# Optimization experiments

Hardware: AMD Instinct MI355X
Metric: run time of the kernel (lower is better)

The kernel has to match this reference:

```python
import jax, jax.numpy as jnp
import numpy as np

OUT_DIM = 336
ALPHA = 1000.0
BETA = 100.0
EPS = 1e-5


def _normalize(x, ref):
    # ref: [B,G,D] -> mean [B,G,1,D]; std is a GLOBAL scalar with ddof=1 (torch.std default)
    d = x - ref[:, :, None, :]
    std = jnp.std(d, ddof=1)
    return d / (std + EPS)


def _tr_embed(my_dim, T):
    # T: [B, in_dim, G, K] channel-first
    B, in_dim, G, K = T.shape
    fd = my_dim // (in_dim * 2)
    feat_range = jnp.arange(fd, dtype=T.dtype)
    dim_embed = jnp.power(jnp.asarray(ALPHA, T.dtype), feat_range / fd)  # [fd]
    t = jnp.transpose(T, (0, 2, 3, 1))                 # [B,G,K,in_dim]
    div = (BETA * t)[..., None] / dim_embed            # [B,G,K,in_dim,fd]
    e = jnp.stack([jnp.sin(div), jnpp_cos(div)], axis=4) if False else jnp.stack([jnp.sin(div), jnp.cos(div)], axis=4)  # [B,G,K,in_dim,2,fd]
    e = e.reshape(B, G, K, in_dim * 2 * fd)            # interleaved as (dim, sin/cos, feat)
    return jnp.transpose(e, (0, 3, 1, 2))              # [B, in_dim*2*fd, G, K]


def setup_inputs() -> dict:
    key = jax.random.key(0)
    k1, k2, k3, k4 = jax.random.split(key, 4)
    B, G, K, C = 8, 1024, 32, 168
    return {
        "lc_xyz": jax.random.normal(k1, (B, G, 3), dtype=jnp.float32),
        "lc_x": jax.random.normal(k2, (B, G, C), dtype=jnp.float32),
        "knn_xyz": jax.random.normal(k3, (B, G, K, 3), dtype=jnp.float32),
        "knn_x": jax.random.normal(k4, (B, G, K, C), dtype=jnp.float32),
    }


def reference(lc_xyz, lc_x, knn_xyz, knn_x):
    B, G, K, C = knn_x.shape
    knn_x_n = _normalize(knn_x, lc_x)          # [B,G,K,C]
    knn_xyz_n = _normalize(knn_xyz, lc_xyz)    # [B,G,K,3]

    lc = jnp.broadcast_to(lc_xyz[:, :, None, :], (B, G, K, 3))
    # channel-first layout as in the torch code
    knn_x_cf = jnp.transpose(knn_x_n, (0, 3, 1, 2))      # [B,C,G,K]
    knn_xyz_cf = jnp.transpose(knn_xyz_n, (0, 3, 1, 2))  # [B,3,G,K]
    lc_cf = jnp.transpose(lc, (0, 3, 1, 2))              # [B,3,G,K]

    cross = jnp.cross(knn_xyz_cf, lc_cf, axis=1)                        # [B,3,G,K]
    dot = jnp.sum(knn_xyz_cf * lc_cf, axis=1, keepdims=True)            # [B,1,G,K]
    emb = jnp.concatenate([knn_xyz_cf, cross, dot], axis=1)             # [B,7,G,K]
    emb = jnp.tile(emb, (1, C // 7, 1, 1))                              # [B,7*(C//7),G,K]
    knn_x_w = jnp.concatenate([knn_x_cf, emb], axis=1)                  # [B,2C,G,K]

    pe = _tr_embed(OUT_DIM, knn_xyz_cf) + _tr_embed(OUT_DIM, lc_cf)     # [B,OUT_DIM,G,K]
    return (knn_x_w + pe) * pe
```

## Files before the change

### kernel.cpp

```cpp
#include <hip/hip_runtime.h>

#define NGQ 1024
#define NKQ 32
#define NCQ 168
#define NOUTC 336
#define NXF 44040192
#define NXYZQ 786432
#define EPSV 1e-5f
#define PIO2 1.5707963267948966f
#define L2A_OVER_FD 0.17796043436f

#define NPART_X 1024
#define NPART_3 32
#define NPART (NPART_X + NPART_3)

#define GRID 512
#define TPB 512
#define NPAIR 4096
#define TSTR 169
#define TILEF (NKQ * TSTR)

__global__ __launch_bounds__(256) void reduce_kernel(
    const float* __restrict__ knn_x, const float* __restrict__ lc_x,
    const float* __restrict__ knn_xyz, const float* __restrict__ lc_xyz,
    float4* __restrict__ part)
{
    float s = 0.f, q = 0.f, s3 = 0.f, q3 = 0.f;
    const int blk = blockIdx.x;
    const int tid = threadIdx.x;

    if (blk < NPART_X) {
        const float4* __restrict__ x4 = (const float4*)knn_x;
        const int n4 = NXF / 4;
        for (int i = blk * 256 + tid; i < n4; i += NPART_X * 256) {
            float4 v = x4[i];
            int bg  = i / 1344;
            int c4  = i - bg * 1344;
            int r42 = c4 % 42;
            float4 l = *(const float4*)(lc_x + (size_t)bg * NCQ + r42 * 4);
            float dx = v.x - l.x, dy = v.y - l.y, dz = v.z - l.z, dw = v.w - l.w;
            s += (dx + dy) + (dz + dw);
            q = fmaf(dx, dx, q); q = fmaf(dy, dy, q);
            q = fmaf(dz, dz, q); q = fmaf(dw, dw, q);
        }
    } else {
        for (int i = (blk - NPART_X) * 256 + tid; i < NXYZQ; i += NPART_3 * 256) {
            float v = knn_xyz[i];
            int bg = i / 96;
            int j  = i % 3;
            float d = v - lc_xyz[bg * 3 + j];
            s3 += d;
            q3 = fmaf(d, d, q3);
        }
    }

    for (int off = 32; off; off >>= 1) {
        s  += __shfl_down(s,  off);
        q  += __shfl_down(q,  off);
        s3 += __shfl_down(s3, off);
        q3 += __shfl_down(q3, off);
    }
    __shared__ float red[4][4];
    int wv = tid >> 6;
    if ((tid & 63) == 0) { red[wv][0] = s; red[wv][1] = q; red[wv][2] = s3; red[wv][3] = q3; }
    __syncthreads();
    if (tid == 0) {
        part[blk] = make_float4(red[0][0] + red[1][0] + red[2][0] + red[3][0],
                                red[0][1] + red[1][1] + red[2][1] + red[3][1],
                                red[0][2] + red[1][2] + red[2][2] + red[3][2],
                                red[0][3] + red[1][3] + red[2][3] + red[3][3]);
    }
}

__global__ __launch_bounds__(TPB, 4) void main_kernel(
    const float* __restrict__ lc_xyz, const float* __restrict__ lc_x,
    const float* __restrict__ knn_xyz, const float* __restrict__ knn_x,
    const float4* __restrict__ part, float* __restrict__ out)
{
    __shared__ float  s_x[2 * TILEF];
    __shared__ float4 s_cc[2 * NOUTC];
    __shared__ float  s_emb[2 * NKQ * 7];
    __shared__ float2 s_so[NOUTC];
    __shared__ float  s_lc[6];
    __shared__ double redd[8][4];
    __shared__ float  s_inv[2];

    const int tid = threadIdx.x;
    const int wv  = tid >> 6;

    {
        double sd = 0.0, qd = 0.0, s3d = 0.0, q3d = 0.0;
        for (int i = tid; i < NPART; i += TPB) {
            float4 p = part[i];
            sd += p.x; qd += p.y; s3d += p.z; q3d += p.w;
        }
        for (int off = 32; off; off >>= 1) {
            sd  += __shfl_down(sd,  off);  qd  += __shfl_down(qd,  off);
            s3d += __shfl_down(s3d, off);  q3d += __shfl_down(q3d, off);
        }
        if ((tid & 63) == 0) { redd[wv][0]=sd; redd[wv][1]=qd; redd[wv][2]=s3d; redd[wv][3]=q3d; }
        __syncthreads();
        if (tid == 0) {
            double S=0,Q=0,S3=0,Q3=0;
            for (int w = 0; w < 8; ++w) { S+=redd[w][0]; Q+=redd[w][1]; S3+=redd[w][2]; Q3+=redd[w][3]; }
            double varx = (Q  - S  * S  / (double)NXF)   / (double)(NXF - 1);
            double var3 = (Q3 - S3 * S3 / (double)NXYZQ) / (double)(NXYZQ - 1);
            s_inv[0] = 1.0f / ((float)sqrt(varx) + EPSV);
            s_inv[1] = 1.0f / ((float)sqrt(var3) + EPSV);
        }
    }
    for (int c = tid; c < NOUTC; c += TPB) {
        int dq = c / 112;
        int r  = c - dq * 112;
        int sf = (r >= 56);
        int f  = sf ? r - 56 : r;
        float scale = 100.f * exp2f(-L2A_OVER_FD * (float)f);
        s_so[c] = make_float2(scale, sf ? PIO2 : 0.f);
    }
    __syncthreads();
    const float inv_sx = s_inv[0];
    const float inv_s3 = s_inv[1];

    const int c0  = tid >> 6;
    const int low = tid & 63;
    const int gg  = low >> 5;
    const int kq  = low & 31;
    const size_t STEPF = (size_t)8 << 15;

    for (int pp = blockIdx.x; pp < NPAIR; pp += GRID) {
        const size_t bg0 = (size_t)pp * 2;
        const int b  = pp >> 9;
        const int g0 = (pp & 511) << 1;

        __syncthreads();
        {
            const float4* __restrict__ src4 = (const float4*)(knn_x + bg0 * (NKQ * NCQ));
            for (int i = tid; i < 2688; i += TPB) {
                float4 v = src4[i];
                int t   = (i >= 1344);
                int rem = i - t * 1344;
                int kk  = rem / 42;
                int c4  = rem - kk * 42;
                float* dst = s_x + t * TILEF + kk * TSTR + c4 * 4;
                dst[0]=v.x; dst[1]=v.y; dst[2]=v.z; dst[3]=v.w;
            }
            if (tid < 6) s_lc[tid] = lc_xyz[bg0 * 3 + tid];
        }
        __syncthreads();

        if (tid < 64) {
            int t = tid >> 5, k = tid & 31;
            float b0=s_lc[t*3+0], b1=s_lc[t*3+1], b2=s_lc[t*3+2];
            const float* kx = knn_xyz + (bg0 + t) * (NKQ * 3) + k * 3;
            float a0=(kx[0]-b0)*inv_s3, a1=(kx[1]-b1)*inv_s3, a2=(kx[2]-b2)*inv_s3;
            float* e = s_emb + t * (NKQ * 7) + k * 7;
            e[0]=a0; e[1]=a1; e[2]=a2;
            e[3]=a1*b2 - a2*b1;
            e[4]=a2*b0 - a0*b2;
            e[5]=a0*b1 - a1*b0;
            e[6]=a0*b0 + a1*b1 + a2*b2;
        }
        for (int i = tid; i < 2 * NOUTC; i += TPB) {
            int t  = (i >= NOUTC);
            int c  = i - t * NOUTC;
            float2 so = s_so[c];
            int dq = c / 112;
            float pelc = __sinf(fmaf(s_lc[t*3 + dq], so.x, so.y));
            float lx   = (c < NCQ) ? lc_x[(bg0 + t) * NCQ + c] : 0.f;
            s_cc[t * NOUTC + c] = make_float4(so.x, so.y, pelc, lx);
        }
        __syncthreads();

        const float*  sx   = s_x   + gg * TILEF + kq * TSTR;
        const float*  se   = s_emb + gg * (NKQ * 7) + kq * 7;
        const float   xn0 = se[0], xn1 = se[1], xn2 = se[2];
        const float4* cc_t = s_cc + gg * NOUTC;
        float* op = out + (size_t)b * (NOUTC * NGQ * NKQ)
                        + ((size_t)g0 << 5) + low + ((size_t)c0 << 15);
        int c = c0;

#define BODY(WEXPR, TT) do { float4 cc = cc_t[c]; float w = (WEXPR); \
        float pe = __sinf(fmaf((TT), cc.x, cc.y)) + cc.z; \
        __builtin_nontemporal_store((w + pe) * pe, op); op += STEPF; c += 8; } while (0)

        #pragma unroll
        for (int j = 0; j < 14; ++j) BODY((sx[c] - cc.w) * inv_sx, xn0);
        #pragma unroll
        for (int j = 0; j < 7;  ++j) BODY((sx[c] - cc.w) * inv_sx, xn1);
        int e7 = (c0 >= 7) ? c0 - 7 : c0;
        #pragma unroll
        for (int j = 0; j < 7;  ++j) { BODY(se[e7], xn1); e7 = (e7 == 6) ? 0 : e7 + 1; }
        #pragma unroll
        for (int j = 0; j < 14; ++j) { BODY(se[e7], xn2); e7 = (e7 == 6) ? 0 : e7 + 1; }
#undef BODY
    }
}

extern "C" void kernel_launch(void* const* d_in, const int* in_sizes, int n_in,
                              void* d_out, int out_size, void* d_ws, size_t ws_size,
                              hipStream_t stream) {
    const float* lc_xyz  = (const float*)d_in[0];
    const float* lc_x    = (const float*)d_in[1];
    const float* knn_xyz = (const float*)d_in[2];
    const float* knn_x   = (const float*)d_in[3];
    float* outp  = (float*)d_out;
    float4* part = (float4*)d_ws;

    reduce_kernel<<<NPART, 256, 0, stream>>>(knn_x, lc_x, knn_xyz, lc_xyz, part);
    main_kernel<<<GRID, TPB, 0, stream>>>(lc_xyz, lc_x, knn_xyz, knn_x, part, outp);
}
```

Measured before the change: 513.1 us.

## Process one point per block with register prefetch of the next tile

Each 256-thread block now handles a single (batch, group) tile at a time instead of a pair, and the launch grows to 2048 blocks with four tiles each. While the current tile is computed, the knn_x, knn_xyz, lc_xyz and lc_x data for the next tile is loaded into registers. This hides global load latency behind the output computation and stores. Output writes switch from nontemporal stores to plain stores. The per-thread register prefetch buffer may limit occupancy, and the plain stores may pollute the cache.

```diff
diff --git a/kernel.cpp b/kernel.cpp
--- a/kernel.cpp
+++ b/kernel.cpp
@@ -14,9 +14,9 @@
 #define NPART_3 32
 #define NPART (NPART_X + NPART_3)
 
-#define GRID 512
-#define TPB 512
-#define NPAIR 4096
+#define GRID2 2048
+#define TPB2 256
+#define NTILE 8192
 #define TSTR 169
 #define TILEF (NKQ * TSTR)
 
@@ -72,17 +72,18 @@
     }
 }
 
-__global__ __launch_bounds__(TPB, 4) void main_kernel(
+__global__ __launch_bounds__(TPB2) void main_kernel(
     const float* __restrict__ lc_xyz, const float* __restrict__ lc_x,
     const float* __restrict__ knn_xyz, const float* __restrict__ knn_x,
     const float4* __restrict__ part, float* __restrict__ out)
 {
-    __shared__ float  s_x[2 * TILEF];
-    __shared__ float4 s_cc[2 * NOUTC];
-    __shared__ float  s_emb[2 * NKQ * 7];
+    __shared__ float  s_x[TILEF];
+    __shared__ float4 s_cc[NOUTC];
     __shared__ float2 s_so[NOUTC];
-    __shared__ float  s_lc[6];
-    __shared__ double redd[8][4];
+    __shared__ float  s_emb[NKQ * 7];
+    __shared__ float  s_kxyz[NKQ * 3];
+    __shared__ float  s_lc[3];
+    __shared__ double redd[4][4];
     __shared__ float  s_inv[2];
 
     const int tid = threadIdx.x;
@@ -90,7 +91,7 @@
 
     {
         double sd = 0.0, qd = 0.0, s3d = 0.0, q3d = 0.0;
-        for (int i = tid; i < NPART; i += TPB) {
+        for (int i = tid; i < NPART; i += TPB2) {
             float4 p = part[i];
             sd += p.x; qd += p.y; s3d += p.z; q3d += p.w;
         }
@@ -102,14 +103,14 @@
         __syncthreads();
         if (tid == 0) {
             double S=0,Q=0,S3=0,Q3=0;
-            for (int w = 0; w < 8; ++w) { S+=redd[w][0]; Q+=redd[w][1]; S3+=redd[w][2]; Q3+=redd[w][3]; }
+            for (int w = 0; w < 4; ++w) { S+=redd[w][0]; Q+=redd[w][1]; S3+=redd[w][2]; Q3+=redd[w][3]; }
             double varx = (Q  - S  * S  / (double)NXF)   / (double)(NXF - 1);
             double var3 = (Q3 - S3 * S3 / (double)NXYZQ) / (double)(NXYZQ - 1);
             s_inv[0] = 1.0f / ((float)sqrt(varx) + EPSV);
             s_inv[1] = 1.0f / ((float)sqrt(var3) + EPSV);
         }
     }
-    for (int c = tid; c < NOUTC; c += TPB) {
+    for (int c = tid; c < NOUTC; c += TPB2) {
         int dq = c / 112;
         int r  = c - dq * 112;
         int sf = (r >= 56);
@@ -121,67 +122,87 @@
     const float inv_sx = s_inv[0];
     const float inv_s3 = s_inv[1];
 
-    const int c0  = tid >> 6;
-    const int low = tid & 63;
-    const int gg  = low >> 5;
-    const int kq  = low & 31;
+    float4 pf[6];
+    float  pf_kx = 0.f, pf_lcx = 0.f, pf_lx = 0.f;
+    int t = blockIdx.x;
+
+    {
+        const float4* __restrict__ s4 = (const float4*)knn_x + (size_t)t * 1344;
+        #pragma unroll
+        for (int j = 0; j < 5; ++j) pf[j] = s4[tid + 256 * j];
+        if (tid < 64)  pf[5]  = s4[tid + 1280];
+        if (tid < 96)  pf_kx  = knn_xyz[(size_t)t * 96 + tid];
+        if (tid < 3)   pf_lcx = lc_xyz[(size_t)t * 3 + tid];
+        if (tid < NCQ) pf_lx  = lc_x[(size_t)t * NCQ + tid];
+    }
+
+    const int c0 = tid >> 5;
+    const int k  = tid & 31;
     const size_t STEPF = (size_t)8 << 15;
 
-    for (int pp = blockIdx.x; pp < NPAIR; pp += GRID) {
-        const size_t bg0 = (size_t)pp * 2;
-        const int b  = pp >> 9;
-        const int g0 = (pp & 511) << 1;
-
-        __syncthreads();
-        {
-            const float4* __restrict__ src4 = (const float4*)(knn_x + bg0 * (NKQ * NCQ));
-            for (int i = tid; i < 2688; i += TPB) {
-                float4 v = src4[i];
-                int t   = (i >= 1344);
-                int rem = i - t * 1344;
-                int kk  = rem / 42;
-                int c4  = rem - kk * 42;
-                float* dst = s_x + t * TILEF + kk * TSTR + c4 * 4;
+    for (int it = 0; it < 4; ++it) {
+        const int tile = t;
+        const int tn   = t + GRID2;
+
+        __syncthreads();
+        #pragma unroll
+        for (int j = 0; j < 6; ++j) {
+            if (j < 5 || tid < 64) {
+                int i  = tid + 256 * j;
+                int kk = i / 42;
+                int c4 = i - kk * 42;
+                float* dst = s_x + kk * TSTR + c4 * 4;
+                float4 v = pf[j];
                 dst[0]=v.x; dst[1]=v.y; dst[2]=v.z; dst[3]=v.w;
             }
-            if (tid < 6) s_lc[tid] = lc_xyz[bg0 * 3 + tid];
-        }
-        __syncthreads();
-
-        if (tid < 64) {
-            int t = tid >> 5, k = tid & 31;
-            float b0=s_lc[t*3+0], b1=s_lc[t*3+1], b2=s_lc[t*3+2];
-            const float* kx = knn_xyz + (bg0 + t) * (NKQ * 3) + k * 3;
-            float a0=(kx[0]-b0)*inv_s3, a1=(kx[1]-b1)*inv_s3, a2=(kx[2]-b2)*inv_s3;
-            float* e = s_emb + t * (NKQ * 7) + k * 7;
+        }
+        if (tid < 96) s_kxyz[tid] = pf_kx;
+        if (tid < 3)  s_lc[tid]  = pf_lcx;
+        const float lxv = pf_lx;
+        __syncthreads();
+
+        if (it < 3) {
+            const float4* __restrict__ s4 = (const float4*)knn_x + (size_t)tn * 1344;
+            #pragma unroll
+            for (int j = 0; j < 5; ++j) pf[j] = s4[tid + 256 * j];
+            if (tid < 64)  pf[5]  = s4[tid + 1280];
+            if (tid < 96)  pf_kx  = knn_xyz[(size_t)tn * 96 + tid];
+            if (tid < 3)   pf_lcx = lc_xyz[(size_t)tn * 3 + tid];
+            if (tid < NCQ) pf_lx  = lc_x[(size_t)tn * NCQ + tid];
+        }
+
+        const float b0 = s_lc[0], b1 = s_lc[1], b2 = s_lc[2];
+        if (tid < NKQ) {
+            float a0 = (s_kxyz[tid*3+0] - b0) * inv_s3;
+            float a1 = (s_kxyz[tid*3+1] - b1) * inv_s3;
+            float a2 = (s_kxyz[tid*3+2] - b2) * inv_s3;
+            float* e = s_emb + tid * 7;
             e[0]=a0; e[1]=a1; e[2]=a2;
             e[3]=a1*b2 - a2*b1;
             e[4]=a2*b0 - a0*b2;
             e[5]=a0*b1 - a1*b0;
             e[6]=a0*b0 + a1*b1 + a2*b2;
         }
-        for (int i = tid; i < 2 * NOUTC; i += TPB) {
-            int t  = (i >= NOUTC);
-            int c  = i - t * NOUTC;
+        for (int c = tid; c < NOUTC; c += TPB2) {
             float2 so = s_so[c];
             int dq = c / 112;
-            float pelc = __sinf(fmaf(s_lc[t*3 + dq], so.x, so.y));
-            float lx   = (c < NCQ) ? lc_x[(bg0 + t) * NCQ + c] : 0.f;
-            s_cc[t * NOUTC + c] = make_float4(so.x, so.y, pelc, lx);
-        }
-        __syncthreads();
-
-        const float*  sx   = s_x   + gg * TILEF + kq * TSTR;
-        const float*  se   = s_emb + gg * (NKQ * 7) + kq * 7;
-        const float   xn0 = se[0], xn1 = se[1], xn2 = se[2];
-        const float4* cc_t = s_cc + gg * NOUTC;
-        float* op = out + (size_t)b * (NOUTC * NGQ * NKQ)
-                        + ((size_t)g0 << 5) + low + ((size_t)c0 << 15);
+            float lcv  = (dq == 0) ? b0 : (dq == 1 ? b1 : b2);
+            float pelc = __sinf(fmaf(lcv, so.x, so.y));
+            float lx   = (c < NCQ) ? lxv : 0.f;
+            s_cc[c] = make_float4(so.x, so.y, pelc, lx);
+        }
+        __syncthreads();
+
+        const float* sx = s_x + k * TSTR;
+        const float* se = s_emb + k * 7;
+        const float xn0 = se[0], xn1 = se[1], xn2 = se[2];
+        float* op = out + (size_t)(tile >> 10) * ((size_t)NOUTC << 15)
+                        + ((size_t)(tile & 1023) << 5) + k + ((size_t)c0 << 15);
         int c = c0;
 
-#define BODY(WEXPR, TT) do { float4 cc = cc_t[c]; float w = (WEXPR); \
+#define BODY(WEXPR, TT) do { float4 cc = s_cc[c]; float w = (WEXPR); \
         float pe = __sinf(fmaf((TT), cc.x, cc.y)) + cc.z; \
-        __builtin_nontemporal_store((w + pe) * pe, op); op += STEPF; c += 8; } while (0)
+        *op = (w + pe) * pe; op += STEPF; c += 8; } while (0)
 
         #pragma unroll
         for (int j = 0; j < 14; ++j) BODY((sx[c] - cc.w) * inv_sx, xn0);
@@ -193,6 +214,8 @@
         #pragma unroll
         for (int j = 0; j < 14; ++j) { BODY(se[e7], xn2); e7 = (e7 == 6) ? 0 : e7 + 1; }
 #undef BODY
+
+        t = tn;
     }
 }
 
@@ -207,5 +230,5 @@
     float4* part = (float4*)d_ws;
 
     reduce_kernel<<<NPART, 256, 0, stream>>>(knn_x, lc_x, knn_xyz, lc_xyz, part);
-    main_kernel<<<GRID, TPB, 0, stream>>>(lc_xyz, lc_x, knn_xyz, knn_x, part, outp);
+    main_kernel<<<GRID2, TPB2, 0, stream>>>(lc_xyz, lc_x, knn_xyz, knn_x, part, outp);
 }
```

Result: slower. 532.3 us (+3.7%).
